# Optimization experiments

Measured on AMD Instinct MI355X. Metric: run time of the kernel, lower is better.

## Reference

```python
import jax, jax.numpy as jnp
import numpy as np

N_EMBD = 1024
N_EXPERTS = 8
TOP_K = 2
D_FF = 4 * N_EMBD


def setup_inputs() -> dict:
    key = jax.random.key(0)
    ks = jax.random.split(key, 6)
    B, S = 4, 2048
    s = 1.0 / np.sqrt(N_EMBD)
    sf = 1.0 / np.sqrt(D_FF)
    x = jax.random.normal(ks[0], (B, S, N_EMBD), dtype=jnp.float32)
    router_w = jax.random.uniform(ks[1], (N_EMBD, N_EXPERTS), minval=-s, maxval=s, dtype=jnp.float32)
    wfc = jax.random.uniform(ks[2], (N_EXPERTS, N_EMBD, D_FF), minval=-s, maxval=s, dtype=jnp.float32)
    bfc = jax.random.uniform(ks[3], (N_EXPERTS, D_FF), minval=-s, maxval=s, dtype=jnp.float32)
    wproj = jax.random.uniform(ks[4], (N_EXPERTS, D_FF, N_EMBD), minval=-sf, maxval=sf, dtype=jnp.float32)
    bproj = jax.random.uniform(ks[5], (N_EXPERTS, N_EMBD), minval=-sf, maxval=sf, dtype=jnp.float32)
    return {"x": x, "router_w": router_w, "wfc": wfc, "bfc": bfc, "wproj": wproj, "bproj": bproj}


def reference(x, router_w, wfc, bfc, wproj, bproj):
    B, S, D = x.shape
    E = wfc.shape[0]
    xf = x.reshape(-1, D)  # [N, D] tokens
    logits = xf @ router_w  # [N, E]
    probs = jax.nn.softmax(logits.astype(jnp.float32), axis=-1)
    w, sel = jax.lax.top_k(probs, TOP_K)  # [N, K]
    w = w / jnp.sum(w, axis=-1, keepdims=True)  # norm_topk_prob
    w = w.astype(x.dtype)
    out = jnp.zeros_like(xf)
    for e in range(E):
        # per-token gate for expert e (0 if not routed here) -- same math as
        # gather -> MLP -> weighted scatter-add in the original
        gate = jnp.sum(jnp.where(sel == e, w, jnp.zeros_like(w)), axis=-1)  # [N]
        h = jax.nn.gelu(xf @ wfc[e] + bfc[e], approximate=False)  # [N, 4D]
        y = h @ wproj[e] + bproj[e]  # [N, D]
        out = out + gate[:, None] * y
    return out.reshape(B, S, D)
```

## Files before the change

### kernel.cpp

```cpp
#include <hip/hip_runtime.h>
#include <hip/hip_bf16.h>


#define N_TOK 8192
#define DMODEL 1024
#define NEXP 8
#define DFF 4096
#define CAP 8192
#define MAXW 136

typedef __attribute__((ext_vector_type(8))) short short8;
typedef __attribute__((ext_vector_type(4))) float f32x4;

#define GLOAD_LDS16(g, l)                                              \
  __builtin_amdgcn_global_load_lds(                                    \
      (const __attribute__((address_space(1))) unsigned int*)(g),      \
      (__attribute__((address_space(3))) unsigned int*)(l), 16, 0, 0)

__device__ __forceinline__ unsigned short f2bf(float f) {
  unsigned u = __float_as_uint(f);
  return (unsigned short)((u + 0x7FFFu + ((u >> 16) & 1u)) >> 16);
}

__device__ __forceinline__ float gelu_f(float v) {
  return 0.5f * v * (1.0f + erff(v * 0.70710678118654752f));
}

__global__ void router_k(const float* __restrict__ x, const float* __restrict__ rw,
                         int* __restrict__ cnt, int* __restrict__ tok,
                         float* __restrict__ gate, unsigned short* __restrict__ xb) {
  int lane = threadIdx.x & 63;
  int t = blockIdx.x * 4 + (threadIdx.x >> 6);
  const float* xr = x + (size_t)t * DMODEL;
  unsigned short* xbr = xb + (size_t)t * DMODEL;
  float p[8];
#pragma unroll
  for (int e = 0; e < 8; ++e) p[e] = 0.0f;
#pragma unroll
  for (int j = 0; j < DMODEL / 64; ++j) {
    int i = lane + j * 64;
    float xv = xr[i];
    xbr[i] = f2bf(xv);
    const float4* r = (const float4*)(rw + (size_t)i * 8);
    float4 a = r[0], b = r[1];
    p[0] += xv * a.x; p[1] += xv * a.y; p[2] += xv * a.z; p[3] += xv * a.w;
    p[4] += xv * b.x; p[5] += xv * b.y; p[6] += xv * b.z; p[7] += xv * b.w;
  }
#pragma unroll
  for (int e = 0; e < 8; ++e) {
#pragma unroll
    for (int off = 32; off; off >>= 1) p[e] += __shfl_xor(p[e], off, 64);
  }
  if (lane == 0) {
    int e1 = 0;
#pragma unroll
    for (int e = 1; e < 8; ++e) if (p[e] > p[e1]) e1 = e;
    int e2 = (e1 == 0) ? 1 : 0;
#pragma unroll
    for (int e = 0; e < 8; ++e) if (e != e1 && p[e] > p[e2]) e2 = e;
    float w1 = 1.0f / (1.0f + expf(p[e2] - p[e1]));
    float w2 = 1.0f - w1;
    int s1 = atomicAdd(&cnt[e1], 1);
    tok[e1 * CAP + s1] = t; gate[e1 * CAP + s1] = w1;
    int s2 = atomicAdd(&cnt[e2], 1);
    tok[e2 * CAP + s2] = t; gate[e2 * CAP + s2] = w2;
  }
}

__global__ void prefix_k(const int* __restrict__ cnt, int* __restrict__ off,
                         int* __restrict__ nwork, int* __restrict__ wl) {
  if (threadIdx.x == 0 && blockIdx.x == 0) {
    int s = 0, n = 0;
    for (int e = 0; e < NEXP; ++e) {
      off[e] = s;
      int ntile = (cnt[e] + 127) >> 7;
      for (int mt = 0; mt < ntile; ++mt) wl[n++] = (e << 16) | mt;
      s += cnt[e];
    }
    nwork[0] = n;
  }
}

__device__ __forceinline__ void cvt_tile(const float* __restrict__ W,
                                         unsigned short* __restrict__ WT,
                                         int K, int N, int b, int t) {
  __shared__ float ls[64][68];
  int nkt = K >> 6, nnt = N >> 6;
  int kt = b % nkt;
  int nt = (b / nkt) % nnt;
  int e = b / (nkt * nnt);
  const float* Wb = W + (size_t)e * K * N + (size_t)(kt * 64) * N + nt * 64;
  int nn = (t & 15) * 4, kr = t >> 4;
#pragma unroll
  for (int i = 0; i < 4; ++i) {
    float4 v = *(const float4*)(Wb + (size_t)(kr + 16 * i) * N + nn);
    *(float4*)&ls[kr + 16 * i][nn] = v;
  }
  __syncthreads();
  int on = t >> 2, kc = (t & 3) * 16;
  unsigned short* dst = WT + (size_t)e * N * K + (size_t)(nt * 64 + on) * K + kt * 64 + kc;
  short8 r0, r1;
#pragma unroll
  for (int j = 0; j < 8; ++j) r0[j] = (short)f2bf(ls[kc + j][on]);
#pragma unroll
  for (int j = 0; j < 8; ++j) r1[j] = (short)f2bf(ls[kc + 8 + j][on]);
  *(short8*)dst = r0;
  *(short8*)(dst + 8) = r1;
}

#define CVT_HALF (NEXP * (DMODEL / 64) * (DFF / 64))
__global__ __launch_bounds__(256) void cvt_both_k(
    const float* __restrict__ wfc, unsigned short* __restrict__ wT1,
    const float* __restrict__ wproj, unsigned short* __restrict__ wT2) {
  int b = blockIdx.x;
  if (b < CVT_HALF) cvt_tile(wfc, wT1, DMODEL, DFF, b, threadIdx.x);
  else cvt_tile(wproj, wT2, DFF, DMODEL, b - CVT_HALF, threadIdx.x);
}

__global__ __launch_bounds__(256) void cvt_wt_k(const float* __restrict__ W,
                                                unsigned short* __restrict__ WT,
                                                int K, int N) {
  cvt_tile(W, WT, K, N, blockIdx.x, threadIdx.x);
}

#define STAGE(buf, kk)                                          \
  do {                                                          \
    GLOAD_LDS16(gA + (kk), &As[buf][tid * 8]);                  \
    GLOAD_LDS16(gB + (kk), &Bs[buf][tid * 8]);                  \
  } while (0)

#define COMPUTE(buf)                                                            \
  do {                                                                          \
    short8 af[4], bfv[2];                                                       \
    _Pragma("unroll") for (int i = 0; i < 4; ++i)                               \
        af[i] = *(const short8*)&As[buf][(wr * 64 + i * 16 + fr) * 32 + co];    \
    _Pragma("unroll") for (int i = 0; i < 2; ++i)                               \
        bfv[i] = *(const short8*)&Bs[buf][(wc * 32 + i * 16 + fr) * 32 + co];   \
    __builtin_amdgcn_s_setprio(1);                                              \
    _Pragma("unroll") for (int mi = 0; mi < 4; ++mi)                            \
        _Pragma("unroll") for (int ni = 0; ni < 2; ++ni)                        \
            acc[mi][ni] = __builtin_amdgcn_mfma_f32_16x16x32_bf16(              \
                af[mi], bfv[ni], acc[mi][ni], 0, 0, 0);                         \
    __builtin_amdgcn_s_setprio(0);                                              \
  } while (0)

#define WAITV(n) asm volatile("s_waitcnt vmcnt(" #n ")" ::: "memory")
#define BAR() __builtin_amdgcn_s_barrier()

#define KLOOP(KTOT)                                                       \
  STAGE(0, 0);                                                            \
  STAGE(1, 32);                                                           \
  STAGE(2, 64);                                                           \
  {                                                                       \
    int k0 = 0;                                                           \
    _Pragma("unroll 1") for (int it = 0; it < ((KTOT) / 32 - 5) / 3; ++it) { \
      WAITV(4); BAR(); COMPUTE(0); BAR(); STAGE(0, k0 + 96);              \
      WAITV(4); BAR(); COMPUTE(1); BAR(); STAGE(1, k0 + 128);             \
      WAITV(4); BAR(); COMPUTE(2); BAR(); STAGE(2, k0 + 160);             \
      k0 += 96;                                                           \
    }                                                                     \
    WAITV(4); BAR(); COMPUTE(0); BAR(); STAGE(0, k0 + 96);                \
    WAITV(4); BAR(); COMPUTE(1); BAR(); STAGE(1, k0 + 128);               \
    WAITV(4); BAR(); COMPUTE(2);                                          \
    WAITV(2); BAR(); COMPUTE(0);                                          \
    WAITV(0); BAR(); COMPUTE(1);                                          \
  }

#define NT1 32
__global__ __launch_bounds__(512, 4) void gemm1a_k(
    const unsigned short* __restrict__ xb, const unsigned short* __restrict__ wT,
    const float* __restrict__ bfc, const int* __restrict__ cnt,
    const int* __restrict__ off, const int* __restrict__ tok,
    const int* __restrict__ nwork, const int* __restrict__ wl,
    unsigned short* __restrict__ h) {
  int bid = (int)(blockIdx.x & 7) * ((int)gridDim.x >> 3) + (int)(blockIdx.x >> 3);
  int widx = bid / NT1;
  int nt = bid % NT1;
  if (widx >= nwork[0]) return;
  int wle = wl[widx];
  int e = wle >> 16;
  int mt = wle & 0xffff;
  int Me = cnt[e];
  int base = off[e];
  int n0 = nt * 128;

  __shared__ __align__(16) unsigned short As[3][128 * 32];
  __shared__ __align__(16) unsigned short Bs[3][128 * 32];

  int tid = threadIdx.x;
  int lane = tid & 63, w = tid >> 6;
  int lc = (((tid & 3) ^ ((tid >> 3) & 3)) * 8);

  int ari = mt * 128 + (tid >> 2);
  int t0 = tok[e * CAP + ((ari < Me) ? ari : (Me - 1))];
  const unsigned short* gA = xb + (size_t)t0 * DMODEL + lc;
  const unsigned short* gB = wT + ((size_t)e * DFF + n0 + (tid >> 2)) * DMODEL + lc;

  int wr = w >> 2, wc = w & 3;
  int g = lane >> 4, fr = lane & 15;
  int co = ((g ^ ((fr >> 1) & 3)) & 3) * 8;

  f32x4 acc[4][2];
#pragma unroll
  for (int i = 0; i < 4; ++i)
#pragma unroll
    for (int j = 0; j < 2; ++j) acc[i][j] = (f32x4)0.0f;

  KLOOP(DMODEL);

#pragma unroll
  for (int mi = 0; mi < 4; ++mi) {
    int rl = wr * 64 + mi * 16 + g * 4;
#pragma unroll
    for (int i = 0; i < 4; ++i) {
      int r = mt * 128 + rl + i;
      if (r < Me) {
        unsigned short* hrow = h + (size_t)(base + r) * DFF;
#pragma unroll
        for (int ni = 0; ni < 2; ++ni) {
          int col = n0 + wc * 32 + ni * 16 + fr;
          float v = acc[mi][ni][i] + bfc[e * DFF + col];
          hrow[col] = f2bf(gelu_f(v));
        }
      }
    }
  }
}

#define NT2 8
__global__ __launch_bounds__(512, 4) void gemm2a_k(
    const unsigned short* __restrict__ h, const unsigned short* __restrict__ wT,
    const float* __restrict__ bproj, const int* __restrict__ cnt,
    const int* __restrict__ off, const int* __restrict__ tok,
    const int* __restrict__ nwork, const int* __restrict__ wl,
    const float* __restrict__ gate, float* __restrict__ out) {
  int bid = (int)(blockIdx.x & 7) * ((int)gridDim.x >> 3) + (int)(blockIdx.x >> 3);
  int widx = bid / NT2;
  int nt = bid % NT2;
  if (widx >= nwork[0]) return;
  int wle = wl[widx];
  int e = wle >> 16;
  int mt = wle & 0xffff;
  int Me = cnt[e];
  int base = off[e];
  int n0 = nt * 128;

  __shared__ __align__(16) unsigned short As[3][128 * 32];
  __shared__ __align__(16) unsigned short Bs[3][128 * 32];

  int tid = threadIdx.x;
  int lane = tid & 63, w = tid >> 6;
  int lc = (((tid & 3) ^ ((tid >> 3) & 3)) * 8);

  const unsigned short* gA = h + (size_t)(base + mt * 128 + (tid >> 2)) * DFF + lc;
  const unsigned short* gB = wT + ((size_t)e * DMODEL + n0 + (tid >> 2)) * DFF + lc;

  int wr = w >> 2, wc = w & 3;
  int g = lane >> 4, fr = lane & 15;
  int co = ((g ^ ((fr >> 1) & 3)) & 3) * 8;

  f32x4 acc[4][2];
#pragma unroll
  for (int i = 0; i < 4; ++i)
#pragma unroll
    for (int j = 0; j < 2; ++j) acc[i][j] = (f32x4)0.0f;

  KLOOP(DFF);

#pragma unroll
  for (int mi = 0; mi < 4; ++mi) {
    int rl = wr * 64 + mi * 16 + g * 4;
#pragma unroll
    for (int i = 0; i < 4; ++i) {
      int r = mt * 128 + rl + i;
      if (r < Me) {
        int tkn = tok[e * CAP + r];
        float gv = gate[e * CAP + r];
        float* orow = out + (size_t)tkn * DMODEL;
#pragma unroll
        for (int ni = 0; ni < 2; ++ni) {
          int col = n0 + wc * 32 + ni * 16 + fr;
          float v = acc[mi][ni][i] + bproj[e * DMODEL + col];
          atomicAdd(orow + col, gv * v);
        }
      }
    }
  }
}

extern "C" void kernel_launch(void* const* d_in, const int* in_sizes, int n_in,
                              void* d_out, int out_size, void* d_ws, size_t ws_size,
                              hipStream_t stream) {
  const float* x = (const float*)d_in[0];
  const float* rw = (const float*)d_in[1];
  const float* wfc = (const float*)d_in[2];
  const float* bfc = (const float*)d_in[3];
  const float* wproj = (const float*)d_in[4];
  const float* bproj = (const float*)d_in[5];
  float* out = (float*)d_out;

  char* ws = (char*)d_ws;
  int* cnt = (int*)ws;
  int* off_ = (int*)(ws + 64);
  int* nwork = (int*)(ws + 128);
  int* wl = (int*)(ws + 256);
  int* tok = (int*)(ws + 4096);
  float* gate = (float*)(ws + 4096 + (size_t)NEXP * CAP * 4);
  size_t HOFF = 4096 + 2 * (size_t)NEXP * CAP * 4;
  unsigned short* h = (unsigned short*)(ws + HOFF);
  size_t HSZ = (size_t)(16384 + 128) * DFF * 2;
  size_t XOFF = HOFF + HSZ;
  size_t WOFF = XOFF + (size_t)N_TOK * DMODEL * 2;
  size_t WSZ = (size_t)NEXP * DFF * DMODEL * 2;
  unsigned short* xb = (unsigned short*)(ws + XOFF);
  unsigned short* wT1 = (unsigned short*)(ws + WOFF);

  hipMemsetAsync(cnt, 0, 128, stream);
  hipMemsetAsync(out, 0, (size_t)out_size * 4, stream);
  router_k<<<N_TOK / 4, 256, 0, stream>>>(x, rw, cnt, tok, gate, xb);
  prefix_k<<<1, 64, 0, stream>>>(cnt, off_, nwork, wl);

  if (ws_size >= WOFF + 2 * WSZ) {
    unsigned short* wT2 = (unsigned short*)(ws + WOFF + WSZ);
    cvt_both_k<<<2 * CVT_HALF, 256, 0, stream>>>(wfc, wT1, wproj, wT2);
    gemm1a_k<<<MAXW * NT1, 512, 0, stream>>>(xb, wT1, bfc, cnt, off_, tok, nwork, wl, h);
    gemm2a_k<<<MAXW * NT2, 512, 0, stream>>>(h, wT2, bproj, cnt, off_, tok, nwork, wl, gate, out);
  } else {
    cvt_wt_k<<<NEXP * (DMODEL / 64) * (DFF / 64), 256, 0, stream>>>(wfc, wT1, DMODEL, DFF);
    gemm1a_k<<<MAXW * NT1, 512, 0, stream>>>(xb, wT1, bfc, cnt, off_, tok, nwork, wl, h);
    cvt_wt_k<<<NEXP * (DFF / 64) * (DMODEL / 64), 256, 0, stream>>>(wproj, wT1, DFF, DMODEL);
    gemm2a_k<<<MAXW * NT2, 512, 0, stream>>>(h, wT1, bproj, cnt, off_, tok, nwork, wl, gate, out);
  }
}
```

Measured before the change: 761.2 us.

## Overlap weight conversion with router and first GEMM via merged launches

Folds the wfc fp32-to-bf16 transpose into the router kernel as extra blocks, and folds the wproj conversion into the first expert GEMM kernel as extra blocks. Each of these blocks converts two tiles, one per 256-thread half, and reuses the GEMM's shared memory. The aim is to overlap memory-bound conversion with router and GEMM work and to cut a kernel launch. The risk is that conversion blocks compete with GEMM blocks for CUs and bandwidth. The swizzled block-id mapping now also spreads conversion blocks across the grid.

```diff
diff --git a/kernel.cpp b/kernel.cpp
--- a/kernel.cpp
+++ b/kernel.cpp
@@ -26,11 +26,48 @@
   return 0.5f * v * (1.0f + erff(v * 0.70710678118654752f));
 }
 
-__global__ void router_k(const float* __restrict__ x, const float* __restrict__ rw,
-                         int* __restrict__ cnt, int* __restrict__ tok,
-                         float* __restrict__ gate, unsigned short* __restrict__ xb) {
+__device__ __forceinline__ void cvt_tile_ls(const float* __restrict__ W,
+                                            unsigned short* __restrict__ WT,
+                                            int K, int N, int b, int t,
+                                            float* __restrict__ ls) {
+  int nkt = K >> 6, nnt = N >> 6;
+  int kt = b % nkt;
+  int nt = (b / nkt) % nnt;
+  int e = b / (nkt * nnt);
+  const float* Wb = W + (size_t)e * K * N + (size_t)(kt * 64) * N + nt * 64;
+  int nn = (t & 15) * 4, kr = t >> 4;
+#pragma unroll
+  for (int i = 0; i < 4; ++i) {
+    float4 v = *(const float4*)(Wb + (size_t)(kr + 16 * i) * N + nn);
+    *(float4*)&ls[(kr + 16 * i) * 68 + nn] = v;
+  }
+  __syncthreads();
+  int on = t >> 2, kc = (t & 3) * 16;
+  unsigned short* dst = WT + (size_t)e * N * K + (size_t)(nt * 64 + on) * K + kt * 64 + kc;
+  short8 r0, r1;
+#pragma unroll
+  for (int j = 0; j < 8; ++j) r0[j] = (short)f2bf(ls[(kc + j) * 68 + on]);
+#pragma unroll
+  for (int j = 0; j < 8; ++j) r1[j] = (short)f2bf(ls[(kc + 8 + j) * 68 + on]);
+  *(short8*)dst = r0;
+  *(short8*)(dst + 8) = r1;
+}
+
+#define RTR_BLKS (N_TOK / 4)
+#define CVT1_BLKS (NEXP * (DMODEL / 64) * (DFF / 64))
+__global__ __launch_bounds__(256) void router_cvt_k(
+    const float* __restrict__ x, const float* __restrict__ rw,
+    int* __restrict__ cnt, int* __restrict__ tok, float* __restrict__ gate,
+    unsigned short* __restrict__ xb,
+    const float* __restrict__ wfc, unsigned short* __restrict__ wT1) {
+  __shared__ float ls[64 * 68];
+  int blk = blockIdx.x;
+  if (blk >= RTR_BLKS) {
+    cvt_tile_ls(wfc, wT1, DMODEL, DFF, blk - RTR_BLKS, threadIdx.x, ls);
+    return;
+  }
   int lane = threadIdx.x & 63;
-  int t = blockIdx.x * 4 + (threadIdx.x >> 6);
+  int t = blk * 4 + (threadIdx.x >> 6);
   const float* xr = x + (size_t)t * DMODEL;
   unsigned short* xbr = xb + (size_t)t * DMODEL;
   float p[8];
@@ -81,46 +118,11 @@
   }
 }
 
-__device__ __forceinline__ void cvt_tile(const float* __restrict__ W,
-                                         unsigned short* __restrict__ WT,
-                                         int K, int N, int b, int t) {
-  __shared__ float ls[64][68];
-  int nkt = K >> 6, nnt = N >> 6;
-  int kt = b % nkt;
-  int nt = (b / nkt) % nnt;
-  int e = b / (nkt * nnt);
-  const float* Wb = W + (size_t)e * K * N + (size_t)(kt * 64) * N + nt * 64;
-  int nn = (t & 15) * 4, kr = t >> 4;
-#pragma unroll
-  for (int i = 0; i < 4; ++i) {
-    float4 v = *(const float4*)(Wb + (size_t)(kr + 16 * i) * N + nn);
-    *(float4*)&ls[kr + 16 * i][nn] = v;
-  }
-  __syncthreads();
-  int on = t >> 2, kc = (t & 3) * 16;
-  unsigned short* dst = WT + (size_t)e * N * K + (size_t)(nt * 64 + on) * K + kt * 64 + kc;
-  short8 r0, r1;
-#pragma unroll
-  for (int j = 0; j < 8; ++j) r0[j] = (short)f2bf(ls[kc + j][on]);
-#pragma unroll
-  for (int j = 0; j < 8; ++j) r1[j] = (short)f2bf(ls[kc + 8 + j][on]);
-  *(short8*)dst = r0;
-  *(short8*)(dst + 8) = r1;
-}
-
-#define CVT_HALF (NEXP * (DMODEL / 64) * (DFF / 64))
-__global__ __launch_bounds__(256) void cvt_both_k(
-    const float* __restrict__ wfc, unsigned short* __restrict__ wT1,
-    const float* __restrict__ wproj, unsigned short* __restrict__ wT2) {
-  int b = blockIdx.x;
-  if (b < CVT_HALF) cvt_tile(wfc, wT1, DMODEL, DFF, b, threadIdx.x);
-  else cvt_tile(wproj, wT2, DFF, DMODEL, b - CVT_HALF, threadIdx.x);
-}
-
 __global__ __launch_bounds__(256) void cvt_wt_k(const float* __restrict__ W,
                                                 unsigned short* __restrict__ WT,
                                                 int K, int N) {
-  cvt_tile(W, WT, K, N, blockIdx.x, threadIdx.x);
+  __shared__ float ls[64 * 68];
+  cvt_tile_ls(W, WT, K, N, blockIdx.x, threadIdx.x, ls);
 }
 
 #define STAGE(buf, kk)                                          \
@@ -166,14 +168,34 @@
     WAITV(0); BAR(); COMPUTE(1);                                          \
   }
 
+typedef unsigned short lds_tile_t[128 * 32];
+
 #define NT1 32
-__global__ __launch_bounds__(512, 4) void gemm1a_k(
+#define G1_BLKS (MAXW * NT1)
+#define CVT2_TILES (NEXP * (DFF / 64) * (DMODEL / 64))
+#define CVT2_BLKS (CVT2_TILES / 2)
+__global__ __launch_bounds__(512, 4) void gemm1cvt_k(
     const unsigned short* __restrict__ xb, const unsigned short* __restrict__ wT,
     const float* __restrict__ bfc, const int* __restrict__ cnt,
     const int* __restrict__ off, const int* __restrict__ tok,
     const int* __restrict__ nwork, const int* __restrict__ wl,
-    unsigned short* __restrict__ h) {
-  int bid = (int)(blockIdx.x & 7) * ((int)gridDim.x >> 3) + (int)(blockIdx.x >> 3);
+    unsigned short* __restrict__ h,
+    const float* __restrict__ wproj, unsigned short* __restrict__ wT2) {
+  __shared__ __align__(16) unsigned char smem[6 * sizeof(lds_tile_t)];
+  lds_tile_t* As = (lds_tile_t*)smem;
+  lds_tile_t* Bs = (lds_tile_t*)(smem + 3 * sizeof(lds_tile_t));
+
+  int half = (int)gridDim.x >> 3;
+  int bid = (int)(blockIdx.x & 7) * half + (int)(blockIdx.x >> 3);
+  int tid = threadIdx.x;
+
+  if (bid >= G1_BLKS) {
+    int b0 = (bid - G1_BLKS) * 2 + (tid >> 8);
+    float* ls = (float*)smem + (tid >> 8) * (64 * 68);
+    cvt_tile_ls(wproj, wT2, DFF, DMODEL, b0, tid & 255, ls);
+    return;
+  }
+
   int widx = bid / NT1;
   int nt = bid % NT1;
   if (widx >= nwork[0]) return;
@@ -184,10 +206,6 @@
   int base = off[e];
   int n0 = nt * 128;
 
-  __shared__ __align__(16) unsigned short As[3][128 * 32];
-  __shared__ __align__(16) unsigned short Bs[3][128 * 32];
-
-  int tid = threadIdx.x;
   int lane = tid & 63, w = tid >> 6;
   int lc = (((tid & 3) ^ ((tid >> 3) & 3)) * 8);
 
@@ -234,6 +252,9 @@
     const int* __restrict__ off, const int* __restrict__ tok,
     const int* __restrict__ nwork, const int* __restrict__ wl,
     const float* __restrict__ gate, float* __restrict__ out) {
+  __shared__ __align__(16) unsigned short As[3][128 * 32];
+  __shared__ __align__(16) unsigned short Bs[3][128 * 32];
+
   int bid = (int)(blockIdx.x & 7) * ((int)gridDim.x >> 3) + (int)(blockIdx.x >> 3);
   int widx = bid / NT2;
   int nt = bid % NT2;
@@ -244,9 +265,6 @@
   int Me = cnt[e];
   int base = off[e];
   int n0 = nt * 128;
-
-  __shared__ __align__(16) unsigned short As[3][128 * 32];
-  __shared__ __align__(16) unsigned short Bs[3][128 * 32];
 
   int tid = threadIdx.x;
   int lane = tid & 63, w = tid >> 6;
@@ -317,18 +335,21 @@
 
   hipMemsetAsync(cnt, 0, 128, stream);
   hipMemsetAsync(out, 0, (size_t)out_size * 4, stream);
-  router_k<<<N_TOK / 4, 256, 0, stream>>>(x, rw, cnt, tok, gate, xb);
-  prefix_k<<<1, 64, 0, stream>>>(cnt, off_, nwork, wl);
 
   if (ws_size >= WOFF + 2 * WSZ) {
     unsigned short* wT2 = (unsigned short*)(ws + WOFF + WSZ);
-    cvt_both_k<<<2 * CVT_HALF, 256, 0, stream>>>(wfc, wT1, wproj, wT2);
-    gemm1a_k<<<MAXW * NT1, 512, 0, stream>>>(xb, wT1, bfc, cnt, off_, tok, nwork, wl, h);
+    router_cvt_k<<<RTR_BLKS + CVT1_BLKS, 256, 0, stream>>>(x, rw, cnt, tok, gate, xb, wfc, wT1);
+    prefix_k<<<1, 64, 0, stream>>>(cnt, off_, nwork, wl);
+    gemm1cvt_k<<<G1_BLKS + CVT2_BLKS, 512, 0, stream>>>(
+        xb, wT1, bfc, cnt, off_, tok, nwork, wl, h, wproj, wT2);
     gemm2a_k<<<MAXW * NT2, 512, 0, stream>>>(h, wT2, bproj, cnt, off_, tok, nwork, wl, gate, out);
   } else {
-    cvt_wt_k<<<NEXP * (DMODEL / 64) * (DFF / 64), 256, 0, stream>>>(wfc, wT1, DMODEL, DFF);
-    gemm1a_k<<<MAXW * NT1, 512, 0, stream>>>(xb, wT1, bfc, cnt, off_, tok, nwork, wl, h);
-    cvt_wt_k<<<NEXP * (DFF / 64) * (DMODEL / 64), 256, 0, stream>>>(wproj, wT1, DFF, DMODEL);
+    router_cvt_k<<<RTR_BLKS, 256, 0, stream>>>(x, rw, cnt, tok, gate, xb, wfc, wT1);
+    prefix_k<<<1, 64, 0, stream>>>(cnt, off_, nwork, wl);
+    cvt_wt_k<<<CVT1_BLKS, 256, 0, stream>>>(wfc, wT1, DMODEL, DFF);
+    gemm1cvt_k<<<G1_BLKS, 512, 0, stream>>>(
+        xb, wT1, bfc, cnt, off_, tok, nwork, wl, h, wproj, wT1);
+    cvt_wt_k<<<CVT2_TILES, 256, 0, stream>>>(wproj, wT1, DFF, DMODEL);
     gemm2a_k<<<MAXW * NT2, 512, 0, stream>>>(h, wT1, bproj, cnt, off_, tok, nwork, wl, gate, out);
   }
 }
```

Result: slower. 896.4 us (+17.8%).
